# Kernel optimization log

Measured on AMD Instinct MI355X. Metric: run time of the kernel, lower is better.

## Reference

```python
import jax, jax.numpy as jnp
import numpy as np

# Clos factorization for in=out=4096, middle_switch_multiplier=4:
BIN, B1, B2, B3, BOUT = 64, 64, 256, 64, 64
B, C, D = 2, 4096, 4096


def setup_inputs() -> dict:
    key = jax.random.key(0)
    ks = jax.random.split(key, 7)
    k = 1.0 / np.sqrt(D)
    x = jax.random.normal(ks[0], (B, C, D), dtype=jnp.float32)
    # kaiming_uniform(a=sqrt(5)) on [bin,b1,b2]-like tensors ~ uniform(-bound, bound)
    w1 = jax.random.uniform(ks[1], (BIN, B1, B2), jnp.float32, -k, k)
    w2 = jax.random.uniform(ks[2], (B1, B2, B3), jnp.float32, -k, k)
    w3 = jax.random.uniform(ks[3], (B2, B3, BOUT), jnp.float32, -k, k)
    bias1 = jax.random.uniform(ks[4], (B1,), jnp.float32, -k, k)
    bias2 = jax.random.uniform(ks[5], (B2,), jnp.float32, -k, k)
    bias3 = jax.random.uniform(ks[6], (B3,), jnp.float32, -k, k)
    return {"x": x, "w1": w1, "w2": w2, "w3": w3,
            "bias1": bias1, "bias2": bias2, "bias3": bias3}


def reference(x, w1, w2, w3, bias1, bias2, bias3):
    b, c, _ = x.shape
    h = x.reshape(b, c, BIN, B1)                      # [b,c,n=bin,r=b1]
    h = jnp.einsum('bcnr,nrm->bcmr', h, w1) + bias1   # [b,c,b2,b1] + bias over b1
    h = jnp.einsum('bcmr,rmn->bcnm', h, w2) + bias2   # [b,c,b3,b2] + bias over b2
    h = jnp.einsum('bcnm,mro->bcor', h, w3) + bias3   # [b,c,bout,b3] + bias over b3
    return h.reshape(b, c, -1)                        # [b,c,out_features]
```

## Files before the change

### kernel.cpp

```cpp
#include <hip/hip_runtime.h>
#include <stdint.h>
#include <stddef.h>

typedef __bf16 bf16_t;
typedef __bf16 bf16x8 __attribute__((ext_vector_type(8)));
typedef __bf16 bf16x4 __attribute__((ext_vector_type(4)));
typedef float f32x4 __attribute__((ext_vector_type(4)));

#define VMW(n) asm volatile("s_waitcnt vmcnt(" #n ")" ::: "memory")
#define LGKM0 asm volatile("s_waitcnt lgkmcnt(0)" ::: "memory")
#define CFENCE asm volatile("" ::: "memory")
#define RAWBAR              \
  do {                      \
    __builtin_amdgcn_s_barrier(); \
    CFENCE;                 \
  } while (0)

__device__ __forceinline__ void gload_lds16(const void* g, void* l) {
  __builtin_amdgcn_global_load_lds(
      (const __attribute__((address_space(1))) uint32_t*)g,
      (__attribute__((address_space(3))) uint32_t*)l, 16, 0, 0);
}

__global__ void prep1_k(const float* __restrict__ w2, const float* __restrict__ w3,
                        float* __restrict__ w2s, bf16_t* __restrict__ w3pt) {
  __shared__ float lds[64][65];
  const int b = blockIdx.x;
  const int t = threadIdx.x;
  if (b < 64) {
    const int r = b, m = t;
    const float4* p = (const float4*)(w2 + ((size_t)(r * 256 + m)) * 64);
    float s = 0.f;
#pragma unroll
    for (int i = 0; i < 16; ++i) {
      float4 v = p[i];
      s += (v.x + v.y) + (v.z + v.w);
    }
    w2s[r * 256 + m] = s;
    return;
  }
  const int b2 = b - 64;
  const int r = b2 & 63;
  const int mt = (b2 >> 6) * 64;
#pragma unroll
  for (int it = 0; it < 16; ++it) {
    int idx = t + it * 256;
    int ml = idx >> 6, o = idx & 63;
    lds[ml][o] = w3[(size_t)(mt + ml) * 4096 + r * 64 + o];
  }
  __syncthreads();
#pragma unroll
  for (int it = 0; it < 16; ++it) {
    int idx = t + it * 256;
    int o = idx >> 6, ml = idx & 63;
    w3pt[(size_t)(o * 64 + r) * 256 + mt + ml] = (bf16_t)lds[ml][o];
  }
}

__global__ void prep2_k(const float* __restrict__ w1, const float* __restrict__ w2s,
                        const float* __restrict__ bias1, const float* __restrict__ bias2,
                        bf16_t* __restrict__ w1t, float* __restrict__ c2) {
  __shared__ float lds[64][65];
  const int b = blockIdx.x;
  const int t = threadIdx.x;
  if (b == 256) {
    float s = 64.f * bias2[t];
#pragma unroll 8
    for (int r = 0; r < 64; ++r) s += bias1[r] * w2s[r * 256 + t];
    c2[t] = s;
    return;
  }
  const int k0 = (b >> 2) * 64;
  const int mt = (b & 3) * 64;
#pragma unroll
  for (int it = 0; it < 16; ++it) {
    int idx = t + it * 256;
    int kl = idx >> 6, ml = idx & 63;
    int k = k0 + kl;
    lds[kl][ml] = w1[(size_t)k * 256 + mt + ml] * w2s[(k & 63) * 256 + mt + ml];
  }
  __syncthreads();
#pragma unroll
  for (int it = 0; it < 16; ++it) {
    int idx = t + it * 256;
    int ml = idx >> 6, kl = idx & 63;
    w1t[(size_t)(mt + ml) * 4096 + k0 + kl] = (bf16_t)lds[kl][ml];
  }
}

__global__ __launch_bounds__(512, 4) void gemm1_k(
    const float* __restrict__ X, const bf16_t* __restrict__ W1T,
    bf16_t* __restrict__ S4) {
  __shared__ __align__(16) bf16_t lA[2][64 * 64];
  __shared__ __align__(16) bf16_t lB[2][256 * 64];
  const int tid = threadIdx.x;
  const int lane = tid & 63;
  const int wv = tid >> 6;
  const int bid = (int)blockIdx.x;
  const int xcd = bid & 7;
  const int rr = bid >> 3;
  const int mtile = xcd * 16 + (rr >> 2);
  const int kh = rr & 3;
  const size_t m0 = (size_t)mtile * 64;
  const int kbase = kh * 1024;
  const int wm = wv >> 2, wn = wv & 3;
  const int r0 = tid >> 4;
  const int f4 = tid & 15;

  f32x4 acc[2][4];
#pragma unroll
  for (int i = 0; i < 2; ++i)
#pragma unroll
    for (int j = 0; j < 4; ++j) acc[i][j] = (f32x4){0.f, 0.f, 0.f, 0.f};

  float4 s0[2], s1[2];

  auto issueA = [&](float4 (&dst)[2], int kt) {
#pragma unroll
    for (int p = 0; p < 2; ++p) {
      int row = r0 + p * 32;
      dst[p] = *(const float4*)(X + (m0 + row) * 4096 + (size_t)(kbase + kt * 64 + f4 * 4));
    }
  };
  auto writeA = [&](const float4 (&src)[2], int buf) {
#pragma unroll
    for (int p = 0; p < 2; ++p) {
      int row = r0 + p * 32;
      int off = row * 128 + ((f4 * 8) ^ ((row & 7) << 4));
      bf16x4 v;
      v[0] = (bf16_t)src[p].x;
      v[1] = (bf16_t)src[p].y;
      v[2] = (bf16_t)src[p].z;
      v[3] = (bf16_t)src[p].w;
      *(bf16x4*)((char*)(&lA[buf][0]) + off) = v;
    }
  };
  auto issueB = [&](int buf, int kt) {
#pragma unroll
    for (int i = 0; i < 4; ++i) {
      int row = wv * 32 + i * 8 + (lane >> 3);
      int srckb = ((lane & 7) * 16) ^ ((row & 7) << 4);
      const char* src = (const char*)W1T + (size_t)row * 8192 + (size_t)(kbase + kt * 64) * 2 + srckb;
      char* dst = (char*)(&lB[buf][0]) + (wv * 32 + i * 8) * 128;
      gload_lds16(src, dst);
    }
  };
  auto compute = [&](int buf) {
#pragma unroll
    for (int kk = 0; kk < 2; ++kk) {
      const int kb = kk * 64 + ((lane >> 4) * 16);
      bf16x8 af[2], bfr[4];
#pragma unroll
      for (int mf = 0; mf < 2; ++mf) {
        int row = wm * 32 + mf * 16 + (lane & 15);
        int off = row * 128 + (kb ^ ((row & 7) << 4));
        af[mf] = *(const bf16x8*)((const char*)(&lA[buf][0]) + off);
      }
#pragma unroll
      for (int nf = 0; nf < 4; ++nf) {
        int row = wn * 64 + nf * 16 + (lane & 15);
        int off = row * 128 + (kb ^ ((row & 7) << 4));
        bfr[nf] = *(const bf16x8*)((const char*)(&lB[buf][0]) + off);
      }
#pragma unroll
      for (int mf = 0; mf < 2; ++mf)
#pragma unroll
        for (int nf = 0; nf < 4; ++nf)
          acc[mf][nf] = __builtin_amdgcn_mfma_f32_16x16x32_bf16(af[mf], bfr[nf], acc[mf][nf], 0, 0, 0);
    }
  };

  issueA(s0, 0);
  CFENCE;
  issueB(0, 0);
  CFENCE;
  issueA(s1, 1);
  CFENCE;
  VMW(6);
  writeA(s0, 0);
  VMW(2);
  LGKM0;
  RAWBAR;

#pragma unroll 1
  for (int kt2 = 0; kt2 < 14; kt2 += 2) {
    issueB(1, kt2 + 1);
    CFENCE;
    issueA(s0, kt2 + 2);
    CFENCE;
    VMW(6);
    writeA(s1, 1);
    compute(0);
    VMW(2);
    LGKM0;
    RAWBAR;
    issueB(0, kt2 + 2);
    CFENCE;
    issueA(s1, kt2 + 3);
    CFENCE;
    VMW(6);
    writeA(s0, 0);
    compute(1);
    VMW(2);
    LGKM0;
    RAWBAR;
  }
  issueB(1, 15);
  CFENCE;
  VMW(4);
  writeA(s1, 1);
  compute(0);
  VMW(0);
  LGKM0;
  RAWBAR;
  compute(1);

#pragma unroll
  for (int nf = 0; nf < 4; ++nf) {
    int col = wn * 64 + nf * 16 + (lane & 15);
#pragma unroll
    for (int mf = 0; mf < 2; ++mf) {
#pragma unroll
      for (int q = 0; q < 4; ++q) {
        int row = wm * 32 + mf * 16 + (lane >> 4) * 4 + q;
        S4[(m0 + row) * 1024 + (size_t)(kh * 256 + col)] = (bf16_t)acc[mf][nf][q];
      }
    }
  }
}

__global__ __launch_bounds__(256) void reduce_k(
    const bf16_t* __restrict__ S4, const float* __restrict__ c2,
    bf16_t* __restrict__ S) {
  const int bid = (int)blockIdx.x;
  const int base = (bid & 7) * 1024 + (bid >> 3) * 8;
  const int t = threadIdx.x;
  const int row = base + (t >> 5);
  const int c8 = (t & 31) << 3;
  float s[8];
  float4 ca = *(const float4*)(c2 + c8);
  float4 cb = *(const float4*)(c2 + c8 + 4);
  s[0] = ca.x; s[1] = ca.y; s[2] = ca.z; s[3] = ca.w;
  s[4] = cb.x; s[5] = cb.y; s[6] = cb.z; s[7] = cb.w;
#pragma unroll
  for (int h = 0; h < 4; ++h) {
    bf16x8 v = *(const bf16x8*)(S4 + (size_t)row * 1024 + h * 256 + c8);
#pragma unroll
    for (int j = 0; j < 8; ++j) s[j] += (float)v[j];
  }
  bf16x8 o;
#pragma unroll
  for (int j = 0; j < 8; ++j) o[j] = (bf16_t)s[j];
  *(bf16x8*)(S + (size_t)row * 256 + c8) = o;
}

__global__ __launch_bounds__(512, 4) void gemm2_k(
    const bf16_t* __restrict__ S, const bf16_t* __restrict__ W3pT,
    const float* __restrict__ bias3, float* __restrict__ OUT) {
  __shared__ __align__(16) bf16_t lA[2][128 * 64];
  __shared__ __align__(16) bf16_t lB[2][128 * 64];
  const int tid = threadIdx.x;
  const int lane = tid & 63;
  const int wv = tid >> 6;
  const int bid = (int)blockIdx.x;
  const int xcd = bid & 7;
  const int rest = bid >> 3;
  const int mt = xcd * 8 + (rest >> 5);
  const int nt = rest & 31;
  const size_t m0 = (size_t)mt * 128;
  const int n0 = nt * 128;
  const int wm = wv >> 2, wn = wv & 3;

  f32x4 acc[4][2];
#pragma unroll
  for (int i = 0; i < 4; ++i)
#pragma unroll
    for (int j = 0; j < 2; ++j) acc[i][j] = (f32x4){0.f, 0.f, 0.f, 0.f};

  auto stage = [&](int buf, int kt) {
#pragma unroll
    for (int p = 0; p < 2; ++p) {
      int row = wv * 8 + (lane >> 3) + p * 64;
      int srckb = ((lane & 7) * 16) ^ ((row & 7) << 4);
      const char* srcA = (const char*)S + (m0 + row) * 512 + (size_t)(kt * 128 + srckb);
      char* dstA = (char*)(&lA[buf][0]) + (wv * 8 + p * 64) * 128;
      gload_lds16(srcA, dstA);
      const char* srcB = (const char*)W3pT + (size_t)(n0 + row) * 512 + (size_t)(kt * 128 + srckb);
      char* dstB = (char*)(&lB[buf][0]) + (wv * 8 + p * 64) * 128;
      gload_lds16(srcB, dstB);
    }
  };
  auto compute = [&](int buf) {
#pragma unroll
    for (int kk = 0; kk < 2; ++kk) {
      const int kb = kk * 64 + ((lane >> 4) * 16);
      bf16x8 af[4], bfr[2];
#pragma unroll
      for (int mf = 0; mf < 4; ++mf) {
        int row = wm * 64 + mf * 16 + (lane & 15);
        int off = row * 128 + (kb ^ ((row & 7) << 4));
        af[mf] = *(const bf16x8*)((const char*)(&lA[buf][0]) + off);
      }
#pragma unroll
      for (int nf = 0; nf < 2; ++nf) {
        int row = wn * 32 + nf * 16 + (lane & 15);
        int off = row * 128 + (kb ^ ((row & 7) << 4));
        bfr[nf] = *(const bf16x8*)((const char*)(&lB[buf][0]) + off);
      }
#pragma unroll
      for (int mf = 0; mf < 4; ++mf)
#pragma unroll
        for (int nf = 0; nf < 2; ++nf)
          acc[mf][nf] = __builtin_amdgcn_mfma_f32_16x16x32_bf16(af[mf], bfr[nf], acc[mf][nf], 0, 0, 0);
    }
  };

  stage(0, 0);
  CFENCE;
  VMW(0);
  RAWBAR;
#pragma unroll 1
  for (int kt = 0; kt < 4; ++kt) {
    int cur = kt & 1;
    if (kt + 1 < 4) {
      stage(cur ^ 1, kt + 1);
      CFENCE;
    }
    compute(cur);
    if (kt + 1 < 4) {
      VMW(0);
      RAWBAR;
    }
  }

#pragma unroll
  for (int nf = 0; nf < 2; ++nf) {
    int jcol = wn * 32 + nf * 16 + (lane & 15);
    float b3 = bias3[jcol & 63];
    int j = n0 + jcol;
#pragma unroll
    for (int mf = 0; mf < 4; ++mf) {
#pragma unroll
      for (int q = 0; q < 4; ++q) {
        size_t row = m0 + (size_t)(wm * 64 + mf * 16 + (lane >> 4) * 4 + q);
        OUT[row * 4096 + j] = acc[mf][nf][q] + b3;
      }
    }
  }
}

extern "C" void kernel_launch(void* const* d_in, const int* in_sizes, int n_in,
                              void* d_out, int out_size, void* d_ws, size_t ws_size,
                              hipStream_t stream) {
  (void)in_sizes; (void)n_in; (void)out_size; (void)ws_size;
  const float* x  = (const float*)d_in[0];
  const float* w1 = (const float*)d_in[1];
  const float* w2 = (const float*)d_in[2];
  const float* w3 = (const float*)d_in[3];
  const float* b1 = (const float*)d_in[4];
  const float* b2 = (const float*)d_in[5];
  const float* b3 = (const float*)d_in[6];
  float* out = (float*)d_out;
  char* ws = (char*)d_ws;

  float*  w2s  = (float*)(ws + 0);
  float*  c2   = (float*)(ws + 65536);
  bf16_t* w1t  = (bf16_t*)(ws + 69632);
  bf16_t* w3pt = (bf16_t*)(ws + 69632 + 2097152);
  bf16_t* S4   = (bf16_t*)(ws + 69632 + 2 * 2097152);
  bf16_t* S    = (bf16_t*)(ws + 69632 + 2 * 2097152 + 16777216);

  prep1_k<<<320, 256, 0, stream>>>(w2, w3, w2s, w3pt);
  prep2_k<<<257, 256, 0, stream>>>(w1, w2s, b1, b2, w1t, c2);
  gemm1_k<<<512, 512, 0, stream>>>(x, w1t, S4);
  reduce_k<<<1024, 256, 0, stream>>>(S4, c2, S);
  gemm2_k<<<2048, 512, 0, stream>>>(S, w3pt, b3, out);
}
```

Before: 107.6 us.

## Enlarge GEMM tiles to 128x256 and restructure prefetch pipelines

gemm1 now computes 128-row M tiles with 256 split-K blocks, and gemm2 computes 128x256 output tiles with 1024 blocks. Each wave holds 4x4 MFMA accumulators, and launch bounds drop to 2 blocks per CU. The larger tiles are meant to raise operand reuse from LDS and global memory. The software pipeline is also reordered so B and A are prefetched two stages ahead, and gemm2 gets a fully unrolled two-stage prefetch. The cost is more registers and LDS per block, lower occupancy, and fewer blocks to balance across the CUs.

After: 104.6 us. 2.7% less time.

```diff
diff --git a/kernel.cpp b/kernel.cpp
--- a/kernel.cpp
+++ b/kernel.cpp
@@ -88,10 +88,10 @@
   }
 }
 
-__global__ __launch_bounds__(512, 4) void gemm1_k(
+__global__ __launch_bounds__(512, 2) void gemm1_k(
     const float* __restrict__ X, const bf16_t* __restrict__ W1T,
     bf16_t* __restrict__ S4) {
-  __shared__ __align__(16) bf16_t lA[2][64 * 64];
+  __shared__ __align__(16) bf16_t lA[2][128 * 64];
   __shared__ __align__(16) bf16_t lB[2][256 * 64];
   const int tid = threadIdx.x;
   const int lane = tid & 63;
@@ -99,34 +99,34 @@
   const int bid = (int)blockIdx.x;
   const int xcd = bid & 7;
   const int rr = bid >> 3;
-  const int mtile = xcd * 16 + (rr >> 2);
-  const int kh = rr & 3;
-  const size_t m0 = (size_t)mtile * 64;
+  const int mtile = xcd * 8 + (rr & 7);
+  const int kh = rr >> 3;
+  const size_t m0 = (size_t)mtile * 128;
   const int kbase = kh * 1024;
   const int wm = wv >> 2, wn = wv & 3;
-  const int r0 = tid >> 4;
-  const int f4 = tid & 15;
-
-  f32x4 acc[2][4];
-#pragma unroll
-  for (int i = 0; i < 2; ++i)
+  const int ar = tid >> 4;
+  const int ac = tid & 15;
+
+  f32x4 acc[4][4];
+#pragma unroll
+  for (int i = 0; i < 4; ++i)
 #pragma unroll
     for (int j = 0; j < 4; ++j) acc[i][j] = (f32x4){0.f, 0.f, 0.f, 0.f};
 
-  float4 s0[2], s1[2];
-
-  auto issueA = [&](float4 (&dst)[2], int kt) {
-#pragma unroll
-    for (int p = 0; p < 2; ++p) {
-      int row = r0 + p * 32;
-      dst[p] = *(const float4*)(X + (m0 + row) * 4096 + (size_t)(kbase + kt * 64 + f4 * 4));
-    }
-  };
-  auto writeA = [&](const float4 (&src)[2], int buf) {
-#pragma unroll
-    for (int p = 0; p < 2; ++p) {
-      int row = r0 + p * 32;
-      int off = row * 128 + ((f4 * 8) ^ ((row & 7) << 4));
+  float4 aX[4], aY[4];
+
+  auto issueA = [&](float4 (&dst)[4], int kt) {
+#pragma unroll
+    for (int p = 0; p < 4; ++p) {
+      int row = ar + p * 32;
+      dst[p] = *(const float4*)(X + (m0 + row) * 4096 + (size_t)(kbase + kt * 64 + ac * 4));
+    }
+  };
+  auto writeA = [&](const float4 (&src)[4], int buf) {
+#pragma unroll
+    for (int p = 0; p < 4; ++p) {
+      int row = ar + p * 32;
+      int off = row * 128 + ((ac * 8) ^ ((row & 7) << 4));
       bf16x4 v;
       v[0] = (bf16_t)src[p].x;
       v[1] = (bf16_t)src[p].y;
@@ -149,10 +149,10 @@
 #pragma unroll
     for (int kk = 0; kk < 2; ++kk) {
       const int kb = kk * 64 + ((lane >> 4) * 16);
-      bf16x8 af[2], bfr[4];
-#pragma unroll
-      for (int mf = 0; mf < 2; ++mf) {
-        int row = wm * 32 + mf * 16 + (lane & 15);
+      bf16x8 af[4], bfr[4];
+#pragma unroll
+      for (int mf = 0; mf < 4; ++mf) {
+        int row = wm * 64 + mf * 16 + (lane & 15);
         int off = row * 128 + (kb ^ ((row & 7) << 4));
         af[mf] = *(const bf16x8*)((const char*)(&lA[buf][0]) + off);
       }
@@ -163,54 +163,53 @@
         bfr[nf] = *(const bf16x8*)((const char*)(&lB[buf][0]) + off);
       }
 #pragma unroll
-      for (int mf = 0; mf < 2; ++mf)
+      for (int mf = 0; mf < 4; ++mf)
 #pragma unroll
         for (int nf = 0; nf < 4; ++nf)
           acc[mf][nf] = __builtin_amdgcn_mfma_f32_16x16x32_bf16(af[mf], bfr[nf], acc[mf][nf], 0, 0, 0);
     }
   };
 
-  issueA(s0, 0);
-  CFENCE;
   issueB(0, 0);
   CFENCE;
-  issueA(s1, 1);
-  CFENCE;
-  VMW(6);
-  writeA(s0, 0);
-  VMW(2);
+  issueA(aX, 0);
+  CFENCE;
+  issueB(1, 1);
+  CFENCE;
+  issueA(aY, 1);
+  CFENCE;
+  VMW(8);
+  writeA(aX, 0);
   LGKM0;
   RAWBAR;
 
 #pragma unroll 1
-  for (int kt2 = 0; kt2 < 14; kt2 += 2) {
-    issueB(1, kt2 + 1);
+  for (int t2 = 0; t2 < 14; t2 += 2) {
+    compute(0);
+    RAWBAR;
+    issueB(0, t2 + 2);
     CFENCE;
-    issueA(s0, kt2 + 2);
+    issueA(aX, t2 + 2);
     CFENCE;
-    VMW(6);
-    writeA(s1, 1);
-    compute(0);
-    VMW(2);
+    VMW(8);
+    writeA(aY, 1);
     LGKM0;
     RAWBAR;
-    issueB(0, kt2 + 2);
+    compute(1);
+    RAWBAR;
+    issueB(1, t2 + 3);
     CFENCE;
-    issueA(s1, kt2 + 3);
+    issueA(aY, t2 + 3);
     CFENCE;
-    VMW(6);
-    writeA(s0, 0);
-    compute(1);
-    VMW(2);
+    VMW(8);
+    writeA(aX, 0);
     LGKM0;
     RAWBAR;
   }
-  issueB(1, 15);
-  CFENCE;
-  VMW(4);
-  writeA(s1, 1);
   compute(0);
+  RAWBAR;
   VMW(0);
+  writeA(aY, 1);
   LGKM0;
   RAWBAR;
   compute(1);
@@ -219,10 +218,10 @@
   for (int nf = 0; nf < 4; ++nf) {
     int col = wn * 64 + nf * 16 + (lane & 15);
 #pragma unroll
-    for (int mf = 0; mf < 2; ++mf) {
+    for (int mf = 0; mf < 4; ++mf) {
 #pragma unroll
       for (int q = 0; q < 4; ++q) {
-        int row = wm * 32 + mf * 16 + (lane >> 4) * 4 + q;
+        int row = wm * 64 + mf * 16 + (lane >> 4) * 4 + q;
         S4[(m0 + row) * 1024 + (size_t)(kh * 256 + col)] = (bf16_t)acc[mf][nf][q];
       }
     }
@@ -254,39 +253,44 @@
   *(bf16x8*)(S + (size_t)row * 256 + c8) = o;
 }
 
-__global__ __launch_bounds__(512, 4) void gemm2_k(
+__global__ __launch_bounds__(512, 2) void gemm2_k(
     const bf16_t* __restrict__ S, const bf16_t* __restrict__ W3pT,
     const float* __restrict__ bias3, float* __restrict__ OUT) {
   __shared__ __align__(16) bf16_t lA[2][128 * 64];
-  __shared__ __align__(16) bf16_t lB[2][128 * 64];
+  __shared__ __align__(16) bf16_t lB[2][256 * 64];
   const int tid = threadIdx.x;
   const int lane = tid & 63;
   const int wv = tid >> 6;
   const int bid = (int)blockIdx.x;
   const int xcd = bid & 7;
   const int rest = bid >> 3;
-  const int mt = xcd * 8 + (rest >> 5);
-  const int nt = rest & 31;
+  const int mt = xcd * 8 + (rest >> 4);
+  const int nt = rest & 15;
   const size_t m0 = (size_t)mt * 128;
-  const int n0 = nt * 128;
+  const int n0 = nt * 256;
   const int wm = wv >> 2, wn = wv & 3;
 
-  f32x4 acc[4][2];
+  f32x4 acc[4][4];
 #pragma unroll
   for (int i = 0; i < 4; ++i)
 #pragma unroll
-    for (int j = 0; j < 2; ++j) acc[i][j] = (f32x4){0.f, 0.f, 0.f, 0.f};
+    for (int j = 0; j < 4; ++j) acc[i][j] = (f32x4){0.f, 0.f, 0.f, 0.f};
 
   auto stage = [&](int buf, int kt) {
 #pragma unroll
-    for (int p = 0; p < 2; ++p) {
-      int row = wv * 8 + (lane >> 3) + p * 64;
+    for (int i = 0; i < 2; ++i) {
+      int row = wv * 16 + i * 8 + (lane >> 3);
       int srckb = ((lane & 7) * 16) ^ ((row & 7) << 4);
-      const char* srcA = (const char*)S + (m0 + row) * 512 + (size_t)(kt * 128 + srckb);
-      char* dstA = (char*)(&lA[buf][0]) + (wv * 8 + p * 64) * 128;
+      const char* srcA = (const char*)S + (m0 + row) * 512 + (size_t)(kt * 128) + srckb;
+      char* dstA = (char*)(&lA[buf][0]) + (wv * 16 + i * 8) * 128;
       gload_lds16(srcA, dstA);
-      const char* srcB = (const char*)W3pT + (size_t)(n0 + row) * 512 + (size_t)(kt * 128 + srckb);
-      char* dstB = (char*)(&lB[buf][0]) + (wv * 8 + p * 64) * 128;
+    }
+#pragma unroll
+    for (int i = 0; i < 4; ++i) {
+      int row = wv * 32 + i * 8 + (lane >> 3);
+      int srckb = ((lane & 7) * 16) ^ ((row & 7) << 4);
+      const char* srcB = (const char*)W3pT + (size_t)(n0 + row) * 512 + (size_t)(kt * 128) + srckb;
+      char* dstB = (char*)(&lB[buf][0]) + (wv * 32 + i * 8) * 128;
       gload_lds16(srcB, dstB);
     }
   };
@@ -294,7 +298,7 @@
 #pragma unroll
     for (int kk = 0; kk < 2; ++kk) {
       const int kb = kk * 64 + ((lane >> 4) * 16);
-      bf16x8 af[4], bfr[2];
+      bf16x8 af[4], bfr[4];
 #pragma unroll
       for (int mf = 0; mf < 4; ++mf) {
         int row = wm * 64 + mf * 16 + (lane & 15);
@@ -302,40 +306,46 @@
         af[mf] = *(const bf16x8*)((const char*)(&lA[buf][0]) + off);
       }
 #pragma unroll
-      for (int nf = 0; nf < 2; ++nf) {
-        int row = wn * 32 + nf * 16 + (lane & 15);
+      for (int nf = 0; nf < 4; ++nf) {
+        int row = wn * 64 + nf * 16 + (lane & 15);
         int off = row * 128 + (kb ^ ((row & 7) << 4));
         bfr[nf] = *(const bf16x8*)((const char*)(&lB[buf][0]) + off);
       }
 #pragma unroll
       for (int mf = 0; mf < 4; ++mf)
 #pragma unroll
-        for (int nf = 0; nf < 2; ++nf)
+        for (int nf = 0; nf < 4; ++nf)
           acc[mf][nf] = __builtin_amdgcn_mfma_f32_16x16x32_bf16(af[mf], bfr[nf], acc[mf][nf], 0, 0, 0);
     }
   };
 
   stage(0, 0);
   CFENCE;
+  stage(1, 1);
+  CFENCE;
+  VMW(6);
+  RAWBAR;
+  compute(0);
+  RAWBAR;
+  stage(0, 2);
+  CFENCE;
+  VMW(6);
+  RAWBAR;
+  compute(1);
+  RAWBAR;
+  stage(1, 3);
+  CFENCE;
+  VMW(6);
+  RAWBAR;
+  compute(0);
+  RAWBAR;
   VMW(0);
   RAWBAR;
-#pragma unroll 1
-  for (int kt = 0; kt < 4; ++kt) {
-    int cur = kt & 1;
-    if (kt + 1 < 4) {
-      stage(cur ^ 1, kt + 1);
-      CFENCE;
-    }
-    compute(cur);
-    if (kt + 1 < 4) {
-      VMW(0);
-      RAWBAR;
-    }
-  }
-
-#pragma unroll
-  for (int nf = 0; nf < 2; ++nf) {
-    int jcol = wn * 32 + nf * 16 + (lane & 15);
+  compute(1);
+
+#pragma unroll
+  for (int nf = 0; nf < 4; ++nf) {
+    int jcol = wn * 64 + nf * 16 + (lane & 15);
     float b3 = bias3[jcol & 63];
     int j = n0 + jcol;
 #pragma unroll
@@ -372,7 +382,7 @@
 
   prep1_k<<<320, 256, 0, stream>>>(w2, w3, w2s, w3pt);
   prep2_k<<<257, 256, 0, stream>>>(w1, w2s, b1, b2, w1t, c2);
-  gemm1_k<<<512, 512, 0, stream>>>(x, w1t, S4);
+  gemm1_k<<<256, 512, 0, stream>>>(x, w1t, S4);
   reduce_k<<<1024, 256, 0, stream>>>(S4, c2, S);
-  gemm2_k<<<2048, 512, 0, stream>>>(S, w3pt, b3, out);
-}
+  gemm2_k<<<1024, 512, 0, stream>>>(S, w3pt, b3, out);
+}
```
